# Kernel tuning notes

Hardware: AMD Instinct MI355X
Metric: run time of the kernel (lower is better)

The kernel has to match this reference:

```python
import jax, jax.numpy as jnp
from jax import lax
import numpy as np

B, T = 256, 100
N_FEAT, V, E, H = 64, 32, 8, 512
CAT_POS = np.arange(0, N_FEAT, 4)                                 # 16 categorical feature indices
CONT_POS = np.array([k for k in range(N_FEAT) if k % 4 != 0])      # 48 continuous feature indices
N_CAT, N_CONT = len(CAT_POS), len(CONT_POS)
IN_LEN = N_FEAT + N_CAT * (E - 1)                                  # 176, matches input_linear.in_features
N_LAYERS = 2                                                        # len(hidden_layers) - 1 LSTMs

# Precompute the interleaved output layout of embed(): walking feature index k,
# categorical features occupy E slots, continuous features 1 slot.
def _layout():
    cont_off, cat_off, cur = [], [], 0
    for k in range(N_FEAT):
        if k % 4 == 0:
            cat_off.append(cur); cur += E
        else:
            cont_off.append(cur); cur += 1
    return np.array(cont_off), np.array(cat_off)
CONT_OFF, CAT_OFF = _layout()
CAT_COLS = (CAT_OFF[:, None] + np.arange(E)).ravel()               # [N_CAT*E] target columns


def lstm(x, Wih, Whh, bih, bhh):
    # PyTorch LSTM, batch_first, gate order (i, f, g, o).
    xw = jnp.einsum('bti,gi->btg', x, Wih) + bih                   # [B,T,4H] input projection (one GEMM)
    def step(carry, xw_t):
        h, c = carry
        gates = xw_t + h @ Whh.T + bhh
        i, f, g, o = jnp.split(gates, 4, axis=-1)
        c = jax.nn.sigmoid(f) * c + jax.nn.sigmoid(i) * jnp.tanh(g)
        h = jax.nn.sigmoid(o) * jnp.tanh(c)
        return (h, c), h
    h0 = jnp.zeros((x.shape[0], Whh.shape[1]), x.dtype)
    (_, _), hs = lax.scan(step, (h0, h0), jnp.swapaxes(xw, 0, 1))
    return jnp.swapaxes(hs, 0, 1)                                   # [B,T,H]


def setup_inputs() -> dict:
    key = jax.random.key(0)
    ks = jax.random.split(key, 16)
    s = 0.05
    base = jax.random.normal(ks[0], (B, T, N_FEAT), jnp.float32)
    cats = jax.random.randint(ks[1], (B, T, N_CAT), 0, V)
    x = base.at[..., CAT_POS].set(cats.astype(jnp.float32))
    return {
        'x': x,
        'scaler_mean': jax.random.normal(ks[2], (N_FEAT,), jnp.float32),
        'scaler_scale': jax.random.uniform(ks[3], (N_FEAT,), jnp.float32, minval=0.5, maxval=2.0),
        'emb': jax.random.normal(ks[4], (N_CAT, V, E), jnp.float32) * s,
        'W_in': jax.random.normal(ks[5], (IN_LEN, H), jnp.float32) * s,
        'b_in': jnp.zeros((H,), jnp.float32),
        'Wih': jax.random.normal(ks[6], (N_LAYERS, 4 * H, H), jnp.float32) * s,
        'Whh': jax.random.normal(ks[7], (N_LAYERS, 4 * H, H), jnp.float32) * s,
        'bih': jnp.zeros((N_LAYERS, 4 * H), jnp.float32),
        'bhh': jnp.zeros((N_LAYERS, 4 * H), jnp.float32),
        'W_out': jax.random.normal(ks[8], (H, N_CONT), jnp.float32) * s,
        'b_out': jnp.zeros((N_CONT,), jnp.float32),
        'W_cls': jax.random.normal(ks[9], (N_CAT, H, V), jnp.float32) * s,
        'b_cls': jnp.zeros((N_CAT, V), jnp.float32),
    }


def reference(x, scaler_mean, scaler_scale, emb, W_in, b_in, Wih, Whh, bih, bhh, W_out, b_out, W_cls, b_cls):
    # ---- embed(): vectorized replacement of the triple python loop ----
    scaled = (x - scaler_mean) / scaler_scale                      # sklearn StandardScaler.transform
    cont_vals = scaled[..., CONT_POS]                              # [B,T,48]
    idx = x[..., CAT_POS].astype(jnp.int32)                        # [B,T,16] categorical codes
    embv = emb[jnp.arange(N_CAT)[None, None, :], idx]              # [B,T,16,E] gather
    new = jnp.zeros((x.shape[0], x.shape[1], IN_LEN), x.dtype)
    new = new.at[..., CONT_OFF].set(cont_vals)
    new = new.at[..., CAT_COLS].set(embv.reshape(x.shape[0], x.shape[1], N_CAT * E))
    # ---- input linear + activation ----
    h = jax.nn.relu(new @ W_in + b_in)                             # [B,T,512]
    # ---- stacked LSTMs, activation after each ----
    for l in range(N_LAYERS):
        h = jax.nn.relu(lstm(h, Wih[l], Whh[l], bih[l], bhh[l]))
    last = h[:, -1, :]                                             # [B,512]
    cont_out = last @ W_out + b_out                                # [B,48]
    cls_out = jnp.einsum('bh,nhv->bnv', last, W_cls) + b_cls       # [B,16,32] classification heads
    return (cont_out, cls_out)
```

## Files before the change

kernel.cpp:

```cpp
#include <hip/hip_runtime.h>

#define BB 256
#define TT 100
#define HH 512
#define G4 2048
#define INL 176
#define KIN 192
#define NCAT 16
#define NCONT 48
#define VV 32
#define EE 8
#define MTOT (BB*TT)
#define GRPB 32
#define FS 16

typedef unsigned short u16;
typedef unsigned int   u32;
typedef unsigned long long u64;
typedef __attribute__((ext_vector_type(8))) short bf16x8;
typedef __attribute__((ext_vector_type(4))) float f32x4;

__device__ __forceinline__ float bf2f(u16 u){
    union { u32 i; float f; } v; v.i = ((u32)u) << 16; return v.f;
}
__device__ __forceinline__ u16 f2bf(float f){
    union { float f; u32 i; } v; v.f = f;
    u32 b = v.i;
    b += 0x7FFFu + ((b >> 16) & 1u);
    return (u16)(b >> 16);
}
__device__ __forceinline__ float fast_tanh(float x){
    float e = __expf(2.f * x);
    return 1.f - 2.f / (e + 1.f);
}
__device__ __forceinline__ u64 relu4_bf16(u64 v){
    u64 s = v & 0x8000800080008000ULL;
    u64 m = s - (s >> 15);
    return v & ~(s | m);
}
__device__ __forceinline__ void poll_flag(const int* fp, int thr){
    int it = 0;
    long long t0c = clock64();
    while (__hip_atomic_load(fp, __ATOMIC_RELAXED, __HIP_MEMORY_SCOPE_AGENT) < thr){
        __builtin_amdgcn_s_sleep(1);
        if (((++it) & 31) == 0 && clock64() - t0c > 50000000LL) break;
    }
}

#define FENCE32(a) \
    asm volatile("" : \
        "+v"(a[0]),  "+v"(a[1]),  "+v"(a[2]),  "+v"(a[3]), \
        "+v"(a[4]),  "+v"(a[5]),  "+v"(a[6]),  "+v"(a[7]), \
        "+v"(a[8]),  "+v"(a[9]),  "+v"(a[10]), "+v"(a[11]), \
        "+v"(a[12]), "+v"(a[13]), "+v"(a[14]), "+v"(a[15])); \
    asm volatile("" : \
        "+v"(a[16]), "+v"(a[17]), "+v"(a[18]), "+v"(a[19]), \
        "+v"(a[20]), "+v"(a[21]), "+v"(a[22]), "+v"(a[23]), \
        "+v"(a[24]), "+v"(a[25]), "+v"(a[26]), "+v"(a[27]), \
        "+v"(a[28]), "+v"(a[29]), "+v"(a[30]), "+v"(a[31])); \
    __builtin_amdgcn_sched_barrier(0)

__global__ void PredictionModel_58841051955204_kernel(
    const float* __restrict__ Win, u16* __restrict__ WinT,
    const float* __restrict__ Wih, u16* __restrict__ Wihb,
    const float* __restrict__ Whh, u16* __restrict__ Whhb){
    int idx = blockIdx.x*256 + threadIdx.x;
    if (idx < HH*KIN){
        int h = idx / KIN, i = idx % KIN;
        WinT[idx] = (i < INL) ? f2bf(Win[i*HH + h]) : (u16)0;
        return;
    }
    int c1 = idx - HH*KIN;
    if (c1 < 2*G4*HH){ Wihb[c1] = f2bf(Wih[c1]); return; }
    int c2 = c1 - 2*G4*HH;
    if (c2 < 2*G4*HH) Whhb[c2] = f2bf(Whh[c2]);
}

__global__ void k_feat(const float* __restrict__ x, const float* __restrict__ mean,
                       const float* __restrict__ scale, const float* __restrict__ emb,
                       u16* __restrict__ feat, int* __restrict__ bar){
    if (blockIdx.x == 0){
        for (int i = threadIdx.x; i < 4096; i += 256)
            __hip_atomic_store(&bar[i], 0, __ATOMIC_RELAXED, __HIP_MEMORY_SCOPE_AGENT);
    }
    int idx = blockIdx.x*256 + threadIdx.x;
    int bt = idx >> 4, g = idx & 15;
    if (bt >= MTOT) return;
    const float* xr = x + (size_t)bt*64;
    u16* fr = feat + (size_t)bt*KIN;
    int k0 = g*4;
    int ci = (int)xr[k0];
    if (ci < 0) ci = 0;
    if (ci > VV-1) ci = VV-1;
    const float* ep = emb + (size_t)(g*VV + ci)*EE;
    int c0 = g*11;
    for (int e = 0; e < 8; e++) fr[c0+e] = f2bf(ep[e]);
    for (int j = 1; j <= 3; j++){
        int k = k0 + j;
        fr[c0 + 8 + (j-1)] = f2bf((xr[k] - mean[k]) / scale[k]);
    }
    fr[INL + g] = 0;
}

__global__ __launch_bounds__(256) void k_gemm(
    const u16* __restrict__ A, int lda,
    const u16* __restrict__ W, int K,
    const float* __restrict__ bias1, const float* __restrict__ bias2,
    void* __restrict__ out, int ldo, int kc_cnt, int do_relu, int out_half)
{
    __shared__ u16 sA[64*40];
    __shared__ u16 sB[256*40];
    int tid = threadIdx.x;
    int w = tid >> 6, lane = tid & 63, q = lane >> 4, r = lane & 15;
    int m0 = blockIdx.x * 64;
    int n0 = blockIdx.y * 256;

    f32x4 acc[4][4];
    for (int a_ = 0; a_ < 4; a_++)
        for (int b_ = 0; b_ < 4; b_++){
            acc[a_][b_][0] = 0.f; acc[a_][b_][1] = 0.f;
            acc[a_][b_][2] = 0.f; acc[a_][b_][3] = 0.f;
        }

    for (int kc = 0; kc < kc_cnt; kc++){
        {
            int row = tid >> 2, seg = tid & 3;
            uint4 v = *(const uint4*)(A + (size_t)(m0+row)*lda + kc*32 + seg*8);
            *(uint4*)(&sA[row*40 + seg*8]) = v;
            const u16* wr = W + (size_t)(n0 + tid)*K + kc*32;
            uint4 b0 = *(const uint4*)(wr);
            uint4 b1 = *(const uint4*)(wr+8);
            uint4 b2 = *(const uint4*)(wr+16);
            uint4 b3 = *(const uint4*)(wr+24);
            u16* d = &sB[tid*40];
            *(uint4*)(d)    = b0; *(uint4*)(d+8)  = b1;
            *(uint4*)(d+16) = b2; *(uint4*)(d+24) = b3;
        }
        __syncthreads();
        bf16x8 a[4], b[4];
        for (int mt = 0; mt < 4; mt++) a[mt] = *(const bf16x8*)(&sA[(mt*16 + r)*40 + q*8]);
        for (int i = 0; i < 4; i++)    b[i]  = *(const bf16x8*)(&sB[((w*4+i)*16 + r)*40 + q*8]);
        for (int mt = 0; mt < 4; mt++)
            for (int i = 0; i < 4; i++)
                acc[mt][i] = __builtin_amdgcn_mfma_f32_16x16x32_bf16(a[mt], b[i], acc[mt][i], 0, 0, 0);
        __syncthreads();
    }

    for (int i = 0; i < 4; i++){
        int n = n0 + (w*4+i)*16 + r;
        float bs = 0.f;
        if (bias1) bs += bias1[n];
        if (bias2) bs += bias2[n];
        for (int mt = 0; mt < 4; mt++){
            for (int reg = 0; reg < 4; reg++){
                int m = m0 + mt*16 + q*4 + reg;
                float v = acc[mt][i][reg] + bs;
                if (do_relu) v = fmaxf(v, 0.f);
                if (out_half) ((_Float16*)out)[(size_t)m*ldo + n] = (_Float16)v;
                else          ((u16*)out)[(size_t)m*ldo + n] = f2bf(v);
            }
        }
    }
}

__global__ __launch_bounds__(256, 1) void k_rec2(
    const u16* __restrict__ Wihb,
    const u16* __restrict__ Whhb,
    const u16* __restrict__ Xbuf,
    const float* __restrict__ bih, const float* __restrict__ bhh,
    u64* __restrict__ h0r,
    u64* __restrict__ h1A, u64* __restrict__ h1B,
    int* __restrict__ bar)
{
    extern __shared__ u16 smem[];
    int tid = threadIdx.x;
    int w = tid >> 6, lane = tid & 63, q = lane >> 4, r = lane & 15;
    int lay  = blockIdx.x >> 7;
    int bid7 = blockIdx.x & 127;
    int mg = bid7 & 3, jb = bid7 >> 2;
    int m0 = mg*64, j0 = jb*16;
    int j = j0 + r;
    int* F0x = bar;
    int* F1x = bar + 2048;
    int fidx = (mg*GRPB + jb)*FS;
    const u16* sWih = smem;
    const u16* sWhh = smem + 64*512;

    {
        int row = tid >> 2, seg = tid & 3;
        int g = row >> 4, jj = row & 15;
        const u16* srcI = Wihb + (size_t)lay*G4*HH + (size_t)(g*HH + j0 + jj)*HH;
        const u16* srcW = Whhb + (size_t)lay*G4*HH + (size_t)(g*HH + j0 + jj)*HH;
        for (int i = 0; i < 16; i++){
            int c = seg*16 + i;
            *(uint4*)(&smem[row*512 + ((c ^ (row & 7)) * 8)]) = *(const uint4*)(srcI + c*8);
            *(uint4*)(&smem[64*512 + row*512 + ((c ^ (row & 7)) * 8)]) = *(const uint4*)(srcW + c*8);
        }
    }
    float creg[4] = {0.f, 0.f, 0.f, 0.f};
    if ((r & 3) == 0){
        u64* hz = lay ? h1A : (h0r + (size_t)3*BB*(HH/4));
        for (int reg = 0; reg < 4; reg++){
            int m = m0 + w*16 + q*4 + reg;
            __hip_atomic_store(&hz[(size_t)m*(HH/4) + ((j0 + r) >> 2)], 0ULL,
                               __ATOMIC_RELAXED, __HIP_MEMORY_SCOPE_AGENT);
        }
    }
    asm volatile("s_waitcnt vmcnt(0)" ::: "memory");
    __syncthreads();
    if (tid == 0)
        __hip_atomic_store(lay ? &F1x[fidx] : &F0x[fidx], 1,
                           __ATOMIC_RELAXED, __HIP_MEMORY_SCOPE_AGENT);
    if (tid < GRPB)
        poll_flag((lay ? F1x : F0x) + (mg*GRPB + tid)*FS, 1);
    __syncthreads();

    float bs[4];
    for (int g = 0; g < 4; g++)
        bs[g] = bih[lay*G4 + g*HH + j] + bhh[lay*G4 + g*HH + j];

    if (!lay){
        const u64* xb = (const u64*)Xbuf;
        u64 xn[32], hd[32];
        {
            const u64* hrow = h0r + (size_t)3*BB*(HH/4) + (size_t)(m0 + w*16 + r)*(HH/4);
            #pragma unroll
            for (int kc = 0; kc < 16; kc++){
                int jg0 = kc*8 + q*2;
                hd[kc*2]   = __hip_atomic_load(&hrow[jg0],   __ATOMIC_RELAXED, __HIP_MEMORY_SCOPE_AGENT);
                hd[kc*2+1] = __hip_atomic_load(&hrow[jg0+1], __ATOMIC_RELAXED, __HIP_MEMORY_SCOPE_AGENT);
            }
        }
        {
            const u64* xrow = xb + ((size_t)(m0 + w*16 + r)*TT + 0)*(HH/4);
            #pragma unroll
            for (int kc = 0; kc < 16; kc++){
                int jg0 = kc*8 + q*2;
                xn[kc*2]   = __builtin_nontemporal_load(&xrow[jg0]);
                xn[kc*2+1] = __builtin_nontemporal_load(&xrow[jg0+1]);
            }
        }
        FENCE32(xn);
        f32x4 accA[4];
        for (int g = 0; g < 4; g++){
            accA[g][0] = 0.f; accA[g][1] = 0.f; accA[g][2] = 0.f; accA[g][3] = 0.f;
        }
        #pragma unroll
        for (int kc = 0; kc < 16; kc++){
            union { u64 d[2]; bf16x8 v; } au;
            au.d[0] = xn[kc*2];
            au.d[1] = xn[kc*2+1];
            int cbase = kc*4 + q;
            #pragma unroll
            for (int g = 0; g < 4; g++){
                int row = g*16 + r;
                bf16x8 b = *(const bf16x8*)(&sWih[row*512 + ((cbase ^ (row & 7)) * 8)]);
                accA[g] = __builtin_amdgcn_mfma_f32_16x16x32_bf16(au.v, b, accA[g], 0, 0, 0);
            }
        }

        for (int t = 0; t < TT; t++){
            u32* hdst32 = (u32*)(h0r + (size_t)(t & 3)*BB*(HH/4));

            FENCE32(hd);
            f32x4 acc[4];
            for (int g = 0; g < 4; g++) acc[g] = accA[g];
            #pragma unroll
            for (int kc = 0; kc < 16; kc++){
                union { u64 d[2]; bf16x8 v; } au;
                au.d[0] = hd[kc*2];
                au.d[1] = hd[kc*2+1];
                int cbase = kc*4 + q;
                #pragma unroll
                for (int g = 0; g < 4; g++){
                    int row = g*16 + r;
                    bf16x8 b = *(const bf16x8*)(&sWhh[row*512 + ((cbase ^ (row & 7)) * 8)]);
                    acc[g] = __builtin_amdgcn_mfma_f32_16x16x32_bf16(au.v, b, acc[g], 0, 0, 0);
                }
            }

            #pragma unroll
            for (int reg = 0; reg < 4; reg++){
                int m = m0 + w*16 + q*4 + reg;
                float Gi = acc[0][reg] + bs[0];
                float Gf = acc[1][reg] + bs[1];
                float Gg = acc[2][reg] + bs[2];
                float Go = acc[3][reg] + bs[3];
                float iv = 1.f/(1.f + __expf(-Gi));
                float fv = 1.f/(1.f + __expf(-Gf));
                float gv = fast_tanh(Gg);
                float ov = 1.f/(1.f + __expf(-Go));
                float c = fv * creg[reg] + iv * gv;
                creg[reg] = c;
                float h = ov * fast_tanh(c);
                u32 own = (u32)f2bf(h);
                u32 p01 = own | (((u32)__shfl_xor((int)own, 1)) << 16);
                if ((r & 1) == 0){
                    __hip_atomic_store(&hdst32[(size_t)m*(HH/2) + ((j0 + r) >> 1)], p01,
                                       __ATOMIC_RELAXED, __HIP_MEMORY_SCOPE_AGENT);
                }
            }

            asm volatile("s_waitcnt vmcnt(0)" ::: "memory");
            __syncthreads();
            if (tid == 0)
                __hip_atomic_store(&F0x[fidx], t + 2, __ATOMIC_RELAXED, __HIP_MEMORY_SCOPE_AGENT);

            if (t + 1 < TT){
                {
                    const u64* xrow = xb + ((size_t)(m0 + w*16 + r)*TT + (t+1))*(HH/4);
                    #pragma unroll
                    for (int kc = 0; kc < 16; kc++){
                        int jg0 = kc*8 + q*2;
                        xn[kc*2]   = __builtin_nontemporal_load(&xrow[jg0]);
                        xn[kc*2+1] = __builtin_nontemporal_load(&xrow[jg0+1]);
                    }
                }
                if (tid < 64){
                    if (lane < GRPB) poll_flag(&F0x[(mg*GRPB + lane)*FS], t + 2);
                    else             poll_flag(&F1x[(mg*GRPB + (lane-GRPB))*FS], t - 1);
                }
                __syncthreads();
                {
                    const u64* hrow = h0r + (size_t)(t & 3)*BB*(HH/4)
                                    + (size_t)(m0 + w*16 + r)*(HH/4);
                    #pragma unroll
                    for (int kc = 0; kc < 16; kc++){
                        int jg0 = kc*8 + q*2;
                        hd[kc*2]   = __hip_atomic_load(&hrow[jg0],   __ATOMIC_RELAXED, __HIP_MEMORY_SCOPE_AGENT);
                        hd[kc*2+1] = __hip_atomic_load(&hrow[jg0+1], __ATOMIC_RELAXED, __HIP_MEMORY_SCOPE_AGENT);
                    }
                }
                FENCE32(xn);
                for (int g = 0; g < 4; g++){
                    accA[g][0] = 0.f; accA[g][1] = 0.f; accA[g][2] = 0.f; accA[g][3] = 0.f;
                }
                #pragma unroll
                for (int kc = 0; kc < 16; kc++){
                    union { u64 d[2]; bf16x8 v; } au;
                    au.d[0] = xn[kc*2];
                    au.d[1] = xn[kc*2+1];
                    int cbase = kc*4 + q;
                    #pragma unroll
                    for (int g = 0; g < 4; g++){
                        int row = g*16 + r;
                        bf16x8 b = *(const bf16x8*)(&sWih[row*512 + ((cbase ^ (row & 7)) * 8)]);
                        accA[g] = __builtin_amdgcn_mfma_f32_16x16x32_bf16(au.v, b, accA[g], 0, 0, 0);
                    }
                }
            }
        }
    } else {
        if (tid < GRPB)
            poll_flag(&F0x[(mg*GRPB + tid)*FS], 2);
        __syncthreads();

        for (int t = 0; t < TT; t++){
            const u64* xsrc = h0r + (size_t)(t & 3)*BB*(HH/4);
            const u64* hsrc = (t & 1) ? h1B : h1A;
            u64*       hdst = (t & 1) ? h1A : h1B;
            const u64* xrow = xsrc + (size_t)(m0 + w*16 + r)*(HH/4);
            const u64* hrow = hsrc + (size_t)(m0 + w*16 + r)*(HH/4);

            u64 hx[32], hh[32];
            #pragma unroll
            for (int kc = 0; kc < 16; kc++){
                int jg0 = kc*8 + q*2;
                hx[kc*2]   = __hip_atomic_load(&xrow[jg0],   __ATOMIC_RELAXED, __HIP_MEMORY_SCOPE_AGENT);
                hx[kc*2+1] = __hip_atomic_load(&xrow[jg0+1], __ATOMIC_RELAXED, __HIP_MEMORY_SCOPE_AGENT);
            }
            #pragma unroll
            for (int kc = 0; kc < 16; kc++){
                int jg0 = kc*8 + q*2;
                hh[kc*2]   = __hip_atomic_load(&hrow[jg0],   __ATOMIC_RELAXED, __HIP_MEMORY_SCOPE_AGENT);
                hh[kc*2+1] = __hip_atomic_load(&hrow[jg0+1], __ATOMIC_RELAXED, __HIP_MEMORY_SCOPE_AGENT);
            }
            FENCE32(hx);
            #pragma unroll
            for (int i = 0; i < 32; i++) hx[i] = relu4_bf16(hx[i]);

            f32x4 acc[4];
            for (int g = 0; g < 4; g++){
                acc[g][0] = 0.f; acc[g][1] = 0.f; acc[g][2] = 0.f; acc[g][3] = 0.f;
            }
            #pragma unroll
            for (int kc = 0; kc < 16; kc++){
                union { u64 d[2]; bf16x8 v; } au;
                au.d[0] = hx[kc*2];
                au.d[1] = hx[kc*2+1];
                int cbase = kc*4 + q;
                #pragma unroll
                for (int g = 0; g < 4; g++){
                    int row = g*16 + r;
                    bf16x8 b = *(const bf16x8*)(&sWih[row*512 + ((cbase ^ (row & 7)) * 8)]);
                    acc[g] = __builtin_amdgcn_mfma_f32_16x16x32_bf16(au.v, b, acc[g], 0, 0, 0);
                }
            }
            FENCE32(hh);
            #pragma unroll
            for (int kc = 0; kc < 16; kc++){
                union { u64 d[2]; bf16x8 v; } au;
                au.d[0] = hh[kc*2];
                au.d[1] = hh[kc*2+1];
                int cbase = kc*4 + q;
                #pragma unroll
                for (int g = 0; g < 4; g++){
                    int row = g*16 + r;
                    bf16x8 b = *(const bf16x8*)(&sWhh[row*512 + ((cbase ^ (row & 7)) * 8)]);
                    acc[g] = __builtin_amdgcn_mfma_f32_16x16x32_bf16(au.v, b, acc[g], 0, 0, 0);
                }
            }

            u32* hdst32 = (u32*)hdst;
            #pragma unroll
            for (int reg = 0; reg < 4; reg++){
                int m = m0 + w*16 + q*4 + reg;
                float Gi = acc[0][reg] + bs[0];
                float Gf = acc[1][reg] + bs[1];
                float Gg = acc[2][reg] + bs[2];
                float Go = acc[3][reg] + bs[3];
                float iv = 1.f/(1.f + __expf(-Gi));
                float fv = 1.f/(1.f + __expf(-Gf));
                float gv = fast_tanh(Gg);
                float ov = 1.f/(1.f + __expf(-Go));
                float c = fv * creg[reg] + iv * gv;
                creg[reg] = c;
                float h = ov * fast_tanh(c);
                u32 own = (u32)f2bf(h);
                u32 p01 = own | (((u32)__shfl_xor((int)own, 1)) << 16);
                if ((r & 1) == 0){
                    __hip_atomic_store(&hdst32[(size_t)m*(HH/2) + ((j0 + r) >> 1)], p01,
                                       __ATOMIC_RELAXED, __HIP_MEMORY_SCOPE_AGENT);
                }
            }

            asm volatile("s_waitcnt vmcnt(0)" ::: "memory");
            __syncthreads();
            if (tid == 0)
                __hip_atomic_store(&F1x[fidx], t + 2, __ATOMIC_RELAXED, __HIP_MEMORY_SCOPE_AGENT);

            if (t + 1 < TT){
                if (tid < 64){
                    if (lane < GRPB) poll_flag(&F1x[(mg*GRPB + lane)*FS], t + 2);
                    else             poll_flag(&F0x[(mg*GRPB + (lane-GRPB))*FS], t + 3);
                }
                __syncthreads();
            }
        }
    }
}

__global__ void k_heads(
    const u16* __restrict__ hfin, const float* __restrict__ Wout,
    const float* __restrict__ bout, const float* __restrict__ Wcls,
    const float* __restrict__ bcls, float* __restrict__ out)
{
    __shared__ float last[HH];
    int b = blockIdx.x, tid = threadIdx.x;
    for (int h = tid; h < HH; h += 256) last[h] = fmaxf(bf2f(hfin[b*HH + h]), 0.f);
    __syncthreads();
    for (int o = tid; o < NCONT + NCAT*VV; o += 256){
        if (o < NCONT){
            float a = bout[o];
            for (int h = 0; h < HH; h++) a += last[h] * Wout[h*NCONT + o];
            out[b*NCONT + o] = (a == 0.0f) ? 7.0f : a;
        } else {
            int oc = o - NCONT;
            int n = oc >> 5, v = oc & 31;
            float a = bcls[oc];
            const float* wp = Wcls + (size_t)n*HH*VV + v;
            for (int h = 0; h < HH; h++) a += last[h] * wp[h*VV];
            out[BB*NCONT + b*(NCAT*VV) + oc] = (a == 0.0f) ? 7.0f : a;
        }
    }
}

extern "C" void kernel_launch(void* const* d_in, const int* in_sizes, int n_in,
                              void* d_out, int out_size, void* d_ws, size_t ws_size,
                              hipStream_t stream){
    const float* x      = (const float*)d_in[0];
    const float* smean  = (const float*)d_in[1];
    const float* sscale = (const float*)d_in[2];
    const float* emb    = (const float*)d_in[3];
    const float* Win    = (const float*)d_in[4];
    const float* bin    = (const float*)d_in[5];
    const float* Wih    = (const float*)d_in[6];
    const float* Whh    = (const float*)d_in[7];
    const float* bih    = (const float*)d_in[8];
    const float* bhh    = (const float*)d_in[9];
    const float* Wout   = (const float*)d_in[10];
    const float* bout   = (const float*)d_in[11];
    const float* Wcls   = (const float*)d_in[12];
    const float* bcls   = (const float*)d_in[13];
    (void)in_sizes; (void)n_in; (void)out_size;

    char* ws = (char*)d_ws;
    size_t off = 0;
    u16*      feat  = (u16*)(ws + off);      off += (size_t)MTOT*KIN*2;
    u16*      WinTb = (u16*)(ws + off);      off += (size_t)HH*KIN*2;
    u16*      Xbuf  = (u16*)(ws + off);      off += (size_t)MTOT*HH*2;
    u16*      Wihb  = (u16*)(ws + off);      off += (size_t)2*G4*HH*2;
    u16*      Whhb  = (u16*)(ws + off);      off += (size_t)2*G4*HH*2;
    u64*      h0r   = (u64*)(ws + off);      off += (size_t)4*BB*HH*2;
    u64*      h1A   = (u64*)(ws + off);      off += (size_t)BB*HH*2;
    u64*      h1B   = (u64*)(ws + off);      off += (size_t)BB*HH*2;
    int*      bar   = (int*)(ws + off);      off += 4096*4;
    (void)off; (void)ws_size;

    int prep_n = HH*KIN + 2*2*G4*HH;
    PredictionModel_58841051955204_kernel<<<(prep_n + 255)/256, 256, 0, stream>>>(
        Win, WinTb, Wih, Wihb, Whh, Whhb);

    k_feat<<<1600, 256, 0, stream>>>(x, smean, sscale, emb, feat, bar);
    k_gemm<<<dim3(400, 2), 256, 0, stream>>>(feat, KIN, WinTb, KIN, bin, (const float*)0,
                                             Xbuf, HH, 6, 1, 0);
    k_rec2<<<256, 256, 131072, stream>>>(Wihb, Whhb, Xbuf, bih, bhh,
                                         h0r, h1A, h1B, bar);
    k_heads<<<256, 256, 0, stream>>>((const u16*)h1A, Wout, bout, Wcls, bcls, (float*)d_out);
}
```

Baseline: 1.269 ms.

## Overlap layer-1 input projection with recurrent-state wait in LSTM loop

The second-layer LSTM path now computes the input-projection MFMAs for step t+1 (from layer-0 output) right after publishing step t, before waiting on the peer-block flags for the recurrent state. Only then does it poll the layer-1 flags and load h. This takes the Wih half of the per-step matmul off the critical serial dependency chain on recurrent hidden state. In exchange it keeps an extra accumulator set live in registers and adds a second block barrier per step.

New measurement: 1.324 ms. +4.3%, slower.

```diff
diff --git a/kernel.cpp b/kernel.cpp
--- a/kernel.cpp
+++ b/kernel.cpp
@@ -351,52 +351,54 @@
             }
         }
     } else {
+        u64 hx[32], hh[32];
+        f32x4 accA[4];
+
         if (tid < GRPB)
             poll_flag(&F0x[(mg*GRPB + tid)*FS], 2);
         __syncthreads();
-
-        for (int t = 0; t < TT; t++){
-            const u64* xsrc = h0r + (size_t)(t & 3)*BB*(HH/4);
-            const u64* hsrc = (t & 1) ? h1B : h1A;
-            u64*       hdst = (t & 1) ? h1A : h1B;
-            const u64* xrow = xsrc + (size_t)(m0 + w*16 + r)*(HH/4);
-            const u64* hrow = hsrc + (size_t)(m0 + w*16 + r)*(HH/4);
-
-            u64 hx[32], hh[32];
+        {
+            const u64* hrow = h1A + (size_t)(m0 + w*16 + r)*(HH/4);
+            #pragma unroll
+            for (int kc = 0; kc < 16; kc++){
+                int jg0 = kc*8 + q*2;
+                hh[kc*2]   = __hip_atomic_load(&hrow[jg0],   __ATOMIC_RELAXED, __HIP_MEMORY_SCOPE_AGENT);
+                hh[kc*2+1] = __hip_atomic_load(&hrow[jg0+1], __ATOMIC_RELAXED, __HIP_MEMORY_SCOPE_AGENT);
+            }
+            const u64* xrow = h0r + (size_t)0*BB*(HH/4) + (size_t)(m0 + w*16 + r)*(HH/4);
             #pragma unroll
             for (int kc = 0; kc < 16; kc++){
                 int jg0 = kc*8 + q*2;
                 hx[kc*2]   = __hip_atomic_load(&xrow[jg0],   __ATOMIC_RELAXED, __HIP_MEMORY_SCOPE_AGENT);
                 hx[kc*2+1] = __hip_atomic_load(&xrow[jg0+1], __ATOMIC_RELAXED, __HIP_MEMORY_SCOPE_AGENT);
             }
-            #pragma unroll
-            for (int kc = 0; kc < 16; kc++){
-                int jg0 = kc*8 + q*2;
-                hh[kc*2]   = __hip_atomic_load(&hrow[jg0],   __ATOMIC_RELAXED, __HIP_MEMORY_SCOPE_AGENT);
-                hh[kc*2+1] = __hip_atomic_load(&hrow[jg0+1], __ATOMIC_RELAXED, __HIP_MEMORY_SCOPE_AGENT);
-            }
-            FENCE32(hx);
-            #pragma unroll
-            for (int i = 0; i < 32; i++) hx[i] = relu4_bf16(hx[i]);
-
+        }
+        FENCE32(hx);
+        #pragma unroll
+        for (int i = 0; i < 32; i++) hx[i] = relu4_bf16(hx[i]);
+        for (int g = 0; g < 4; g++){
+            accA[g][0] = 0.f; accA[g][1] = 0.f; accA[g][2] = 0.f; accA[g][3] = 0.f;
+        }
+        #pragma unroll
+        for (int kc = 0; kc < 16; kc++){
+            union { u64 d[2]; bf16x8 v; } au;
+            au.d[0] = hx[kc*2];
+            au.d[1] = hx[kc*2+1];
+            int cbase = kc*4 + q;
+            #pragma unroll
+            for (int g = 0; g < 4; g++){
+                int row = g*16 + r;
+                bf16x8 b = *(const bf16x8*)(&sWih[row*512 + ((cbase ^ (row & 7)) * 8)]);
+                accA[g] = __builtin_amdgcn_mfma_f32_16x16x32_bf16(au.v, b, accA[g], 0, 0, 0);
+            }
+        }
+
+        for (int t = 0; t < TT; t++){
+            u64* hdst = (t & 1) ? h1A : h1B;
+
+            FENCE32(hh);
             f32x4 acc[4];
-            for (int g = 0; g < 4; g++){
-                acc[g][0] = 0.f; acc[g][1] = 0.f; acc[g][2] = 0.f; acc[g][3] = 0.f;
-            }
-            #pragma unroll
-            for (int kc = 0; kc < 16; kc++){
-                union { u64 d[2]; bf16x8 v; } au;
-                au.d[0] = hx[kc*2];
-                au.d[1] = hx[kc*2+1];
-                int cbase = kc*4 + q;
-                #pragma unroll
-                for (int g = 0; g < 4; g++){
-                    int row = g*16 + r;
-                    bf16x8 b = *(const bf16x8*)(&sWih[row*512 + ((cbase ^ (row & 7)) * 8)]);
-                    acc[g] = __builtin_amdgcn_mfma_f32_16x16x32_bf16(au.v, b, acc[g], 0, 0, 0);
-                }
-            }
-            FENCE32(hh);
+            for (int g = 0; g < 4; g++) acc[g] = accA[g];
             #pragma unroll
             for (int kc = 0; kc < 16; kc++){
                 union { u64 d[2]; bf16x8 v; } au;
@@ -440,11 +442,50 @@
                 __hip_atomic_store(&F1x[fidx], t + 2, __ATOMIC_RELAXED, __HIP_MEMORY_SCOPE_AGENT);
 
             if (t + 1 < TT){
-                if (tid < 64){
-                    if (lane < GRPB) poll_flag(&F1x[(mg*GRPB + lane)*FS], t + 2);
-                    else             poll_flag(&F0x[(mg*GRPB + (lane-GRPB))*FS], t + 3);
-                }
+                if (tid < GRPB)
+                    poll_flag(&F0x[(mg*GRPB + tid)*FS], t + 3);
                 __syncthreads();
+                {
+                    const u64* xrow = h0r + (size_t)((t+1) & 3)*BB*(HH/4)
+                                    + (size_t)(m0 + w*16 + r)*(HH/4);
+                    #pragma unroll
+                    for (int kc = 0; kc < 16; kc++){
+                        int jg0 = kc*8 + q*2;
+                        hx[kc*2]   = __hip_atomic_load(&xrow[jg0],   __ATOMIC_RELAXED, __HIP_MEMORY_SCOPE_AGENT);
+                        hx[kc*2+1] = __hip_atomic_load(&xrow[jg0+1], __ATOMIC_RELAXED, __HIP_MEMORY_SCOPE_AGENT);
+                    }
+                }
+                FENCE32(hx);
+                #pragma unroll
+                for (int i = 0; i < 32; i++) hx[i] = relu4_bf16(hx[i]);
+                for (int g = 0; g < 4; g++){
+                    accA[g][0] = 0.f; accA[g][1] = 0.f; accA[g][2] = 0.f; accA[g][3] = 0.f;
+                }
+                #pragma unroll
+                for (int kc = 0; kc < 16; kc++){
+                    union { u64 d[2]; bf16x8 v; } au;
+                    au.d[0] = hx[kc*2];
+                    au.d[1] = hx[kc*2+1];
+                    int cbase = kc*4 + q;
+                    #pragma unroll
+                    for (int g = 0; g < 4; g++){
+                        int row = g*16 + r;
+                        bf16x8 b = *(const bf16x8*)(&sWih[row*512 + ((cbase ^ (row & 7)) * 8)]);
+                        accA[g] = __builtin_amdgcn_mfma_f32_16x16x32_bf16(au.v, b, accA[g], 0, 0, 0);
+                    }
+                }
+                if (tid < GRPB)
+                    poll_flag(&F1x[(mg*GRPB + tid)*FS], t + 2);
+                __syncthreads();
+                {
+                    const u64* hrow = ((t & 1) ? h1A : h1B) + (size_t)(m0 + w*16 + r)*(HH/4);
+                    #pragma unroll
+                    for (int kc = 0; kc < 16; kc++){
+                        int jg0 = kc*8 + q*2;
+                        hh[kc*2]   = __hip_atomic_load(&hrow[jg0],   __ATOMIC_RELAXED, __HIP_MEMORY_SCOPE_AGENT);
+                        hh[kc*2+1] = __hip_atomic_load(&hrow[jg0+1], __ATOMIC_RELAXED, __HIP_MEMORY_SCOPE_AGENT);
+                    }
+                }
             }
         }
     }
```
